# Kernel tuning notes

Hardware: AMD Instinct MI355X
Metric: run time of the kernel (lower is better)

Reference implementation:

```python
import jax, jax.numpy as jnp
import numpy as np

N_TABLES = 26
VOCAB = 100000
D = 64          # m_spa
B = 16384
L = 4           # fixed pooling factor (uniform offsets)
LN_BOT = [13, 512, 256, 64]
LN_TOP = [415, 512, 256, 1]


def setup_inputs() -> dict:
    key = jax.random.key(0)
    ks = jax.random.split(key, 20)
    inp = {}
    inp["dense_x"] = jax.random.uniform(ks[0], (B, LN_BOT[0]), dtype=jnp.float32)
    # offsets: uniform bags of length L (EmbeddingBag offsets per table)
    inp["lS_o"] = jnp.tile(jnp.arange(B, dtype=jnp.int64) * L, (N_TABLES, 1))
    inp["lS_i"] = jax.random.randint(ks[1], (N_TABLES, B * L), 0, VOCAB, dtype=jnp.int64)
    # embedding tables, uniform(-sqrt(1/n), sqrt(1/n)) as in create_emb
    bound = np.sqrt(1.0 / VOCAB)
    inp["emb"] = jax.random.uniform(ks[2], (N_TABLES, VOCAB, D), dtype=jnp.float32,
                                     minval=-bound, maxval=bound)
    # MLP params, normal init as in create_mlp
    def mk_mlp(ln, k0):
        Ws, bs = [], []
        for i in range(len(ln) - 1):
            n, m = ln[i], ln[i + 1]
            kw, kb = jax.random.split(jax.random.fold_in(k0, i))
            Ws.append(jax.random.normal(kw, (m, n), dtype=jnp.float32) * np.sqrt(2.0 / (m + n)))
            bs.append(jax.random.normal(kb, (m,), dtype=jnp.float32) * np.sqrt(1.0 / m))
        return Ws, bs
    bW, bb = mk_mlp(LN_BOT, ks[3])
    tW, tb = mk_mlp(LN_TOP, ks[4])
    for i in range(3):
        inp[f"bot_W{i}"], inp[f"bot_b{i}"] = bW[i], bb[i]
        inp[f"top_W{i}"], inp[f"top_b{i}"] = tW[i], tb[i]
    return inp


def _lower_tri_pairs(n):
    # li/lj from interact_features with offset=0: all (i, j) with j < i
    li = np.array([i for i in range(n) for j in range(i)])
    lj = np.array([j for i in range(n) for j in range(i)])
    return li, lj


def dlrm_forward(dense_x, lS_i, emb, bot_W, bot_b, top_W, top_b):
    # bottom MLP: Linear + ReLU (sigmoid_bot = -1)
    x = dense_x
    for W, b in zip(bot_W, bot_b):
        x = jax.nn.relu(x @ W.T + b)
    # EmbeddingBag sum pooling: gather rows then sum over bag (fixed L)
    idx = lS_i.reshape(N_TABLES, B, L)                 # [T,B,L]
    # vmap over tables: emb[t][idx[t]] -> [B,L,D] -> sum -> [B,D]
    ly = jax.vmap(lambda tbl, ix: tbl[ix].sum(axis=1))(emb, idx)  # [T,B,D]
    # dot interaction: T = [x] + ly along feature axis -> [B, 1+T, D]
    Tmat = jnp.concatenate([x[:, None, :], jnp.transpose(ly, (1, 0, 2))], axis=1)
    Z = jnp.einsum("bid,bjd->bij", Tmat, Tmat)         # [B, 27, 27]
    li, lj = _lower_tri_pairs(Tmat.shape[1])
    Zflat = Z[:, li, lj]                                # [B, 351]
    R = jnp.concatenate([x, Zflat], axis=1)             # [B, 415]
    # top MLP: ReLU, ReLU, Sigmoid (sigmoid_top = 2)
    z = R
    for i, (W, b) in enumerate(zip(top_W, top_b)):
        z = z @ W.T + b
        z = jax.nn.sigmoid(z) if i == len(top_W) - 1 else jax.nn.relu(z)
    return z  # loss_threshold == 0 -> no clamp


def reference(dense_x, lS_o, lS_i, emb,
              bot_W0, bot_b0, bot_W1, bot_b1, bot_W2, bot_b2,
              top_W0, top_b0, top_W1, top_b1, top_W2, top_b2):
    # lS_o encodes uniform bags of length L; structure is honored via reshape.
    del lS_o
    return dlrm_forward(dense_x, lS_i, emb,
                        [bot_W0, bot_W1, bot_W2], [bot_b0, bot_b1, bot_b2],
                        [top_W0, top_W1, top_W2], [top_b0, top_b1, top_b2])
```

## Files before the change

### kernel.cpp

```cpp
#include <hip/hip_runtime.h>
#include <hip/hip_bf16.h>
#include <cmath>

#define BATCH   16384
#define NT      26
#define VOCAB_N 100000
#define EMB_D   64
#define LOOK    4

typedef __attribute__((ext_vector_type(8))) short  short8;
typedef __attribute__((ext_vector_type(4))) float  float4v;

#define GLOBAL_AS __attribute__((address_space(1)))
#define LDS_AS    __attribute__((address_space(3)))

static __device__ __forceinline__ short f32_to_bf16_bits(float f) {
    unsigned u = __builtin_bit_cast(unsigned, f);
    unsigned r = (u + 0x7fffu + ((u >> 16) & 1u)) >> 16;
    return (short)r;
}
static __device__ __forceinline__ float bf16_bits_to_f32(short s) {
    return __builtin_bit_cast(float, ((unsigned)(unsigned short)s) << 16);
}

__global__ __launch_bounds__(256) void conv_all(
    const float* __restrict__ bW1, const float* __restrict__ bW2,
    const float* __restrict__ tW0, const float* __restrict__ tW1,
    __hip_bfloat16* __restrict__ wb1, __hip_bfloat16* __restrict__ wb2,
    __hip_bfloat16* __restrict__ wt0, __hip_bfloat16* __restrict__ wt1)
{
    int i = blockIdx.x * 256 + threadIdx.x;
    if (i < 131072) { wb1[i] = __float2bfloat16(bW1[i]); return; }
    i -= 131072;
    if (i < 16384)  { wb2[i] = __float2bfloat16(bW2[i]); return; }
    i -= 16384;
    if (i < 212992) {
        int r = i / 416, k = i % 416;
        wt0[i] = __float2bfloat16(k < 415 ? tW0[(size_t)r * 415 + k] : 0.f);
        return;
    }
    i -= 212992;
    if (i < 131072) wt1[i] = __float2bfloat16(tW1[i]);
}

__global__ __launch_bounds__(256) void gemm_f32_k13(
    const float* __restrict__ X, const float* __restrict__ W,
    const float* __restrict__ bias, __hip_bfloat16* __restrict__ Y,
    int M, int N, int K)
{
    constexpr int BM = 128, BN = 128, BK = 16, TM = 8, TN = 8, PAD = 4;
    __shared__ __align__(16) float Xs[BK][BM + PAD];
    __shared__ __align__(16) float Ws[BK][BN + PAD];

    const int tid = threadIdx.x;
    const int tx  = tid % (BN / TN);
    const int ty  = tid / (BN / TN);
    const int m0  = blockIdx.y * BM;
    const int n0  = blockIdx.x * BN;

    float acc[TM][TN];
    #pragma unroll
    for (int i = 0; i < TM; i++)
        #pragma unroll
        for (int j = 0; j < TN; j++) acc[i][j] = 0.f;

    for (int k0 = 0; k0 < K; k0 += BK) {
        for (int idx = tid; idx < BM * BK; idx += 256) {
            int r = idx / BK, k = idx % BK, gk = k0 + k;
            Xs[k][r] = (gk < K) ? X[(size_t)(m0 + r) * K + gk] : 0.f;
        }
        for (int idx = tid; idx < BN * BK; idx += 256) {
            int r = idx / BK, k = idx % BK, gk = k0 + k;
            Ws[k][r] = (gk < K) ? W[(size_t)(n0 + r) * K + gk] : 0.f;
        }
        __syncthreads();
        #pragma unroll
        for (int kk = 0; kk < BK; kk++) {
            float a[TM], bb[TN];
            #pragma unroll
            for (int i = 0; i < TM; i++) a[i] = Xs[kk][ty * TM + i];
            #pragma unroll
            for (int j = 0; j < TN; j++) bb[j] = Ws[kk][tx * TN + j];
            #pragma unroll
            for (int i = 0; i < TM; i++)
                #pragma unroll
                for (int j = 0; j < TN; j++)
                    acc[i][j] += a[i] * bb[j];
        }
        __syncthreads();
    }
    #pragma unroll
    for (int i = 0; i < TM; i++) {
        int m = m0 + ty * TM + i;
        #pragma unroll
        for (int j = 0; j < TN; j++) {
            int n = n0 + tx * TN + j;
            float v = fmaxf(acc[i][j] + bias[n], 0.f);
            Y[(size_t)m * N + n] = __float2bfloat16(v);
        }
    }
}

template<int BN, int WM, int WN, int RELU, int OUT_BF16>
__global__ __launch_bounds__(256) void mfma_gemm(
    const short* __restrict__ A, const short* __restrict__ W,
    const float* __restrict__ bias, void* __restrict__ Y,
    int M, int N, int K)
{
    constexpr int BM = 128, BK = 32;
    constexpr int FM = BM / WM / 16;
    constexpr int FN = BN / WN / 16;
    constexpr int ACH = (BM * BK * 2) / 1024;
    constexpr int BCH = (BN * BK * 2) / 1024;

    __shared__ short As[BM * BK];
    __shared__ short Bs[BN * BK];

    const int tid  = threadIdx.x;
    const int wave = tid >> 6;
    const int lane = tid & 63;
    const int wm   = wave / WN;
    const int wn   = wave % WN;
    const int m0   = blockIdx.y * BM;
    const int n0   = blockIdx.x * BN;

    const int r16 = lane >> 2;
    const int c16 = (lane & 3) * 8;

    float4v acc[FM][FN];
    #pragma unroll
    for (int i = 0; i < FM; i++)
        #pragma unroll
        for (int j = 0; j < FN; j++) acc[i][j] = (float4v)(0.f);

    for (int k0 = 0; k0 < K; k0 += BK) {
        #pragma unroll
        for (int c = 0; c < ACH / 4; c++) {
            int chunk = wave * (ACH / 4) + c;
            int row   = chunk * 16 + r16;
            const short* src = A + (size_t)(m0 + row) * K + k0 + c16;
            __builtin_amdgcn_global_load_lds(
                (const GLOBAL_AS void*)src,
                (LDS_AS void*)(As + chunk * 512), 16, 0, 0);
        }
        #pragma unroll
        for (int c = 0; c < BCH / 4; c++) {
            int chunk = wave * (BCH / 4) + c;
            int row   = chunk * 16 + r16;
            const short* src = W + (size_t)(n0 + row) * K + k0 + c16;
            __builtin_amdgcn_global_load_lds(
                (const GLOBAL_AS void*)src,
                (LDS_AS void*)(Bs + chunk * 512), 16, 0, 0);
        }
        __syncthreads();

        short8 a_frag[FM], b_frag[FN];
        const int kq = (lane >> 4) * 8;
        #pragma unroll
        for (int fi = 0; fi < FM; fi++) {
            int m_local = wm * (BM / WM) + fi * 16 + (lane & 15);
            a_frag[fi] = *(const short8*)(As + m_local * BK + kq);
        }
        #pragma unroll
        for (int fj = 0; fj < FN; fj++) {
            int n_local = wn * (BN / WN) + fj * 16 + (lane & 15);
            b_frag[fj] = *(const short8*)(Bs + n_local * BK + kq);
        }
        #pragma unroll
        for (int fi = 0; fi < FM; fi++)
            #pragma unroll
            for (int fj = 0; fj < FN; fj++)
                acc[fi][fj] = __builtin_amdgcn_mfma_f32_16x16x32_bf16(
                    a_frag[fi], b_frag[fj], acc[fi][fj], 0, 0, 0);

        __syncthreads();
    }

    #pragma unroll
    for (int fi = 0; fi < FM; fi++) {
        #pragma unroll
        for (int fj = 0; fj < FN; fj++) {
            int col   = n0 + wn * (BN / WN) + fj * 16 + (lane & 15);
            int rbase = m0 + wm * (BM / WM) + fi * 16 + (lane >> 4) * 4;
            float bv  = bias[col];
            #pragma unroll
            for (int r = 0; r < 4; r++) {
                float v = acc[fi][fj][r] + bv;
                if (RELU) v = fmaxf(v, 0.f);
                if (OUT_BF16)
                    ((__hip_bfloat16*)Y)[(size_t)(rbase + r) * N + col] =
                        __float2bfloat16(v);
                else
                    ((float*)Y)[(size_t)(rbase + r) * N + col] = v;
            }
        }
    }
}

#define TS 68

__global__ __launch_bounds__(256) void interact_kernel(
    const float* __restrict__ x2,
    const int*   __restrict__ lS_i,
    const float* __restrict__ emb,
    __hip_bfloat16* __restrict__ R)
{
    __shared__ __align__(16) float T[32 * TS];
    __shared__ int sidx[NT * LOOK];

    const int b   = blockIdx.x;
    const int tid = threadIdx.x;

    if (tid < NT * LOOK) {
        int tb = tid >> 2, l = tid & 3;
        sidx[tid] = lS_i[(size_t)tb * (BATCH * LOOK) + (size_t)b * LOOK + l];
    }
    if (tid < 16) {
        *(float4*)(&T[tid * 4]) = *(const float4*)(x2 + (size_t)b * EMB_D + tid * 4);
    }
    for (int i = 27 * TS + tid; i < 32 * TS; i += 256) T[i] = 0.f;
    __syncthreads();

    const int c4 = (tid & 15) * 4;
    #pragma unroll
    for (int it = 0; it < 2; ++it) {
        int tb = (tid >> 4) + it * 16;
        if (tb < NT) {
            float4 s = {0.f, 0.f, 0.f, 0.f};
            #pragma unroll
            for (int l = 0; l < LOOK; l++) {
                int row = sidx[tb * LOOK + l];
                float4 v = *(const float4*)(emb +
                    ((size_t)tb * VOCAB_N + row) * EMB_D + c4);
                s.x += v.x; s.y += v.y; s.z += v.z; s.w += v.w;
            }
            *(float4*)(&T[(tb + 1) * TS + c4]) = s;
        }
    }
    __syncthreads();

    const int wave = tid >> 6;
    const int lane = tid & 63;
    __hip_bfloat16* Rb = R + (size_t)b * 416;

    if (wave < 3) {
        const int ti = (wave == 0) ? 0 : 1;
        const int tj = (wave == 2) ? 1 : 0;

        short8 fhi[2][2], flo[2][2];
        const int r  = lane & 15;
        const int kq = (lane >> 4) * 8;
        #pragma unroll
        for (int rt = 0; rt < 2; rt++) {
            #pragma unroll
            for (int kk = 0; kk < 2; kk++) {
                const float* src = &T[(rt * 16 + r) * TS + kk * 32 + kq];
                float4 v0 = *(const float4*)(src);
                float4 v1 = *(const float4*)(src + 4);
                float vv[8] = {v0.x, v0.y, v0.z, v0.w, v1.x, v1.y, v1.z, v1.w};
                short8 h, l;
                #pragma unroll
                for (int j = 0; j < 8; j++) {
                    short hb = f32_to_bf16_bits(vv[j]);
                    float hf = bf16_bits_to_f32(hb);
                    short lb = f32_to_bf16_bits(vv[j] - hf);
                    h[j] = hb; l[j] = lb;
                }
                fhi[rt][kk] = h; flo[rt][kk] = l;
            }
        }

        float4v acc = (float4v)(0.f);
        #pragma unroll
        for (int kk = 0; kk < 2; kk++) {
            acc = __builtin_amdgcn_mfma_f32_16x16x32_bf16(
                      fhi[ti][kk], fhi[tj][kk], acc, 0, 0, 0);
            acc = __builtin_amdgcn_mfma_f32_16x16x32_bf16(
                      fhi[ti][kk], flo[tj][kk], acc, 0, 0, 0);
            acc = __builtin_amdgcn_mfma_f32_16x16x32_bf16(
                      flo[ti][kk], fhi[tj][kk], acc, 0, 0, 0);
        }

        const int gj = tj * 16 + (lane & 15);
        #pragma unroll
        for (int rr = 0; rr < 4; rr++) {
            int gi = ti * 16 + (lane >> 4) * 4 + rr;
            if (gi < NT + 1 && gi > gj) {
                int p = gi * (gi - 1) / 2 + gj;
                Rb[64 + p] = __float2bfloat16(acc[rr]);
            }
        }
    } else {
        Rb[lane] = __float2bfloat16(T[lane]);
        if (lane == 0) Rb[415] = __float2bfloat16(0.f);
    }
}

__global__ __launch_bounds__(256) void top_final(
    const float* __restrict__ z1, const float* __restrict__ W2,
    const float* __restrict__ b2, float* __restrict__ out)
{
    const int wave = threadIdx.x >> 6;
    const int lane = threadIdx.x & 63;
    const int b = blockIdx.x * 4 + wave;

    float s = 0.f;
    #pragma unroll
    for (int q = 0; q < 4; q++) {
        int k = q * 64 + lane;
        s += z1[(size_t)b * 256 + k] * W2[k];
    }
    #pragma unroll
    for (int off = 32; off; off >>= 1) s += __shfl_down(s, off, 64);
    if (lane == 0) out[b] = 1.f / (1.f + expf(-(s + b2[0])));
}

extern "C" void kernel_launch(void* const* d_in, const int* in_sizes, int n_in,
                              void* d_out, int out_size, void* d_ws, size_t ws_size,
                              hipStream_t stream)
{
    const float* dense = (const float*)d_in[0];
    const int*   lS_i  = (const int*)d_in[2];
    const float* emb   = (const float*)d_in[3];
    const float* bW0 = (const float*)d_in[4];  const float* bb0 = (const float*)d_in[5];
    const float* tW0 = (const float*)d_in[6];  const float* tb0 = (const float*)d_in[7];
    const float* bW1 = (const float*)d_in[8];  const float* bb1 = (const float*)d_in[9];
    const float* tW1 = (const float*)d_in[10]; const float* tb1 = (const float*)d_in[11];
    const float* bW2 = (const float*)d_in[12]; const float* bb2 = (const float*)d_in[13];
    const float* tW2 = (const float*)d_in[14]; const float* tb2 = (const float*)d_in[15];
    float* out = (float*)d_out;

    char* p = (char*)d_ws;
    __hip_bfloat16* x0_bf = (__hip_bfloat16*)p;  p += (size_t)BATCH * 512 * 2;
    __hip_bfloat16* x1_bf = (__hip_bfloat16*)p;  p += (size_t)BATCH * 256 * 2;
    float*          x2_f  = (float*)p;           p += (size_t)BATCH * 64  * 4;
    __hip_bfloat16* R_bf  = (__hip_bfloat16*)p;  p += (size_t)BATCH * 416 * 2;
    __hip_bfloat16* z0_bf = (__hip_bfloat16*)p;  p += (size_t)BATCH * 512 * 2;
    float*          z1_f  = (float*)p;           p += (size_t)BATCH * 256 * 4;
    __hip_bfloat16* wb1   = (__hip_bfloat16*)p;  p += (size_t)256 * 512 * 2;
    __hip_bfloat16* wb2   = (__hip_bfloat16*)p;  p += (size_t)64  * 256 * 2;
    __hip_bfloat16* wt0   = (__hip_bfloat16*)p;  p += (size_t)512 * 416 * 2;
    __hip_bfloat16* wt1   = (__hip_bfloat16*)p;  p += (size_t)256 * 512 * 2;

    dim3 blk(256);

    conv_all<<<dim3(1920), blk, 0, stream>>>(bW1, bW2, tW0, tW1, wb1, wb2, wt0, wt1);

    gemm_f32_k13<<<dim3(512 / 128, BATCH / 128), blk, 0, stream>>>(
        dense, bW0, bb0, x0_bf, BATCH, 512, 13);
    mfma_gemm<128, 2, 2, 1, 1><<<dim3(256 / 128, BATCH / 128), blk, 0, stream>>>(
        (const short*)x0_bf, (const short*)wb1, bb1, x1_bf, BATCH, 256, 512);
    mfma_gemm<64, 4, 1, 1, 0><<<dim3(1, BATCH / 128), blk, 0, stream>>>(
        (const short*)x1_bf, (const short*)wb2, bb2, x2_f, BATCH, 64, 256);

    interact_kernel<<<dim3(BATCH), blk, 0, stream>>>(x2_f, lS_i, emb, R_bf);

    mfma_gemm<128, 2, 2, 1, 1><<<dim3(512 / 128, BATCH / 128), blk, 0, stream>>>(
        (const short*)R_bf, (const short*)wt0, tb0, z0_bf, BATCH, 512, 416);
    mfma_gemm<128, 2, 2, 1, 0><<<dim3(256 / 128, BATCH / 128), blk, 0, stream>>>(
        (const short*)z0_bf, (const short*)wt1, tb1, z1_f, BATCH, 256, 512);
    top_final<<<dim3(BATCH / 4), blk, 0, stream>>>(z1_f, tW2, tb2, out);
}
```

Baseline: 895.9 us.

## Fuse bottom-MLP last layer into interaction and top layer 1 into final

```diff
diff --git a/kernel.cpp b/kernel.cpp
--- a/kernel.cpp
+++ b/kernel.cpp
@@ -200,13 +200,17 @@
 #define TS 68
 
 __global__ __launch_bounds__(256) void interact_kernel(
-    const float* __restrict__ x2,
+    const short* __restrict__ x1,
+    const short* __restrict__ wb2,
+    const float* __restrict__ bb2,
     const int*   __restrict__ lS_i,
     const float* __restrict__ emb,
     __hip_bfloat16* __restrict__ R)
 {
     __shared__ __align__(16) float T[32 * TS];
     __shared__ int sidx[NT * LOOK];
+    __shared__ __align__(16) short x1row[256];
+    __shared__ __align__(16) float red[64][4];
 
     const int b   = blockIdx.x;
     const int tid = threadIdx.x;
@@ -215,27 +219,67 @@
         int tb = tid >> 2, l = tid & 3;
         sidx[tid] = lS_i[(size_t)tb * (BATCH * LOOK) + (size_t)b * LOOK + l];
     }
-    if (tid < 16) {
-        *(float4*)(&T[tid * 4]) = *(const float4*)(x2 + (size_t)b * EMB_D + tid * 4);
+    if (tid >= 128 && tid < 160) {
+        int o = (tid - 128) * 8;
+        *(short8*)(&x1row[o]) = *(const short8*)(x1 + (size_t)b * 256 + o);
     }
     for (int i = 27 * TS + tid; i < 32 * TS; i += 256) T[i] = 0.f;
     __syncthreads();
 
-    const int c4 = (tid & 15) * 4;
-    #pragma unroll
-    for (int it = 0; it < 2; ++it) {
-        int tb = (tid >> 4) + it * 16;
-        if (tb < NT) {
-            float4 s = {0.f, 0.f, 0.f, 0.f};
-            #pragma unroll
-            for (int l = 0; l < LOOK; l++) {
-                int row = sidx[tb * LOOK + l];
-                float4 v = *(const float4*)(emb +
-                    ((size_t)tb * VOCAB_N + row) * EMB_D + c4);
-                s.x += v.x; s.y += v.y; s.z += v.z; s.w += v.w;
-            }
-            *(float4*)(&T[(tb + 1) * TS + c4]) = s;
-        }
+    const int c4  = (tid & 15) * 4;
+    const int tb0 = tid >> 4;
+    const int tb1 = tb0 + 16;
+    float4 g[8];
+    #pragma unroll
+    for (int l = 0; l < LOOK; l++) {
+        int row = sidx[tb0 * LOOK + l];
+        g[l] = *(const float4*)(emb + ((size_t)tb0 * VOCAB_N + row) * EMB_D + c4);
+    }
+    if (tb1 < NT) {
+        #pragma unroll
+        for (int l = 0; l < LOOK; l++) {
+            int row = sidx[tb1 * LOOK + l];
+            g[4 + l] = *(const float4*)(emb + ((size_t)tb1 * VOCAB_N + row) * EMB_D + c4);
+        }
+    }
+
+    {
+        const int d = tid & 63, q = tid >> 6;
+        const short* wrow = wb2 + d * 256 + q * 64;
+        float p = 0.f;
+        #pragma unroll
+        for (int c = 0; c < 8; c++) {
+            short8 w  = *(const short8*)(wrow + c * 8);
+            short8 xv = *(const short8*)(&x1row[q * 64 + c * 8]);
+            #pragma unroll
+            for (int j = 0; j < 8; j++)
+                p += bf16_bits_to_f32(xv[j]) * bf16_bits_to_f32(w[j]);
+        }
+        red[d][q] = p;
+    }
+
+    {
+        float4 s = g[0];
+        s.x += g[1].x + g[2].x + g[3].x;
+        s.y += g[1].y + g[2].y + g[3].y;
+        s.z += g[1].z + g[2].z + g[3].z;
+        s.w += g[1].w + g[2].w + g[3].w;
+        *(float4*)(&T[(tb0 + 1) * TS + c4]) = s;
+        if (tb1 < NT) {
+            float4 t = g[4];
+            t.x += g[5].x + g[6].x + g[7].x;
+            t.y += g[5].y + g[6].y + g[7].y;
+            t.z += g[5].z + g[6].z + g[7].z;
+            t.w += g[5].w + g[6].w + g[7].w;
+            *(float4*)(&T[(tb1 + 1) * TS + c4]) = t;
+        }
+    }
+    __syncthreads();
+
+    if (tid < 64) {
+        float4 r4 = *(const float4*)(&red[tid][0]);
+        float v = r4.x + r4.y + r4.z + r4.w + bb2[tid];
+        T[tid] = fmaxf(v, 0.f);
     }
     __syncthreads();
 
@@ -296,23 +340,99 @@
     }
 }
 
-__global__ __launch_bounds__(256) void top_final(
-    const float* __restrict__ z1, const float* __restrict__ W2,
-    const float* __restrict__ b2, float* __restrict__ out)
-{
-    const int wave = threadIdx.x >> 6;
-    const int lane = threadIdx.x & 63;
-    const int b = blockIdx.x * 4 + wave;
-
-    float s = 0.f;
-    #pragma unroll
-    for (int q = 0; q < 4; q++) {
-        int k = q * 64 + lane;
-        s += z1[(size_t)b * 256 + k] * W2[k];
-    }
-    #pragma unroll
-    for (int off = 32; off; off >>= 1) s += __shfl_down(s, off, 64);
-    if (lane == 0) out[b] = 1.f / (1.f + expf(-(s + b2[0])));
+__global__ __launch_bounds__(256) void top1_final(
+    const short* __restrict__ A,
+    const short* __restrict__ W,
+    const float* __restrict__ bias,
+    const float* __restrict__ W2,
+    const float* __restrict__ b2,
+    float* __restrict__ out)
+{
+    constexpr int BM = 64, BN = 256, BK = 32, K = 512;
+    __shared__ short As[BM * BK];
+    __shared__ short Bs[BN * BK];
+    __shared__ __align__(16) float red[64][4];
+
+    const int tid  = threadIdx.x;
+    const int wave = tid >> 6;
+    const int lane = tid & 63;
+    const int m0   = blockIdx.x * BM;
+
+    const int r16 = lane >> 2;
+    const int c16 = (lane & 3) * 8;
+
+    float4v acc[4][4];
+    #pragma unroll
+    for (int i = 0; i < 4; i++)
+        #pragma unroll
+        for (int j = 0; j < 4; j++) acc[i][j] = (float4v)(0.f);
+
+    for (int k0 = 0; k0 < K; k0 += BK) {
+        {
+            int row = wave * 16 + r16;
+            const short* src = A + (size_t)(m0 + row) * K + k0 + c16;
+            __builtin_amdgcn_global_load_lds(
+                (const GLOBAL_AS void*)src,
+                (LDS_AS void*)(As + wave * 512), 16, 0, 0);
+        }
+        #pragma unroll
+        for (int c = 0; c < 4; c++) {
+            int chunk = wave * 4 + c;
+            int row   = chunk * 16 + r16;
+            const short* src = W + (size_t)row * K + k0 + c16;
+            __builtin_amdgcn_global_load_lds(
+                (const GLOBAL_AS void*)src,
+                (LDS_AS void*)(Bs + chunk * 512), 16, 0, 0);
+        }
+        __syncthreads();
+
+        short8 a_frag[4], b_frag[4];
+        const int kq = (lane >> 4) * 8;
+        #pragma unroll
+        for (int fi = 0; fi < 4; fi++) {
+            int m_local = fi * 16 + (lane & 15);
+            a_frag[fi] = *(const short8*)(As + m_local * BK + kq);
+        }
+        #pragma unroll
+        for (int fj = 0; fj < 4; fj++) {
+            int n_local = wave * 64 + fj * 16 + (lane & 15);
+            b_frag[fj] = *(const short8*)(Bs + n_local * BK + kq);
+        }
+        #pragma unroll
+        for (int fi = 0; fi < 4; fi++)
+            #pragma unroll
+            for (int fj = 0; fj < 4; fj++)
+                acc[fi][fj] = __builtin_amdgcn_mfma_f32_16x16x32_bf16(
+                    a_frag[fi], b_frag[fj], acc[fi][fj], 0, 0, 0);
+
+        __syncthreads();
+    }
+
+    #pragma unroll
+    for (int fi = 0; fi < 4; fi++) {
+        #pragma unroll
+        for (int rr = 0; rr < 4; rr++) {
+            float s = 0.f;
+            #pragma unroll
+            for (int fj = 0; fj < 4; fj++) {
+                int col = wave * 64 + fj * 16 + (lane & 15);
+                float v = fmaxf(acc[fi][fj][rr] + bias[col], 0.f);
+                s += v * W2[col];
+            }
+            s += __shfl_xor(s, 1, 64);
+            s += __shfl_xor(s, 2, 64);
+            s += __shfl_xor(s, 4, 64);
+            s += __shfl_xor(s, 8, 64);
+            if ((lane & 15) == 0)
+                red[fi * 16 + (lane >> 4) * 4 + rr][wave] = s;
+        }
+    }
+    __syncthreads();
+    if (tid < 64) {
+        float4 r4 = *(const float4*)(&red[tid][0]);
+        float s = r4.x + r4.y + r4.z + r4.w + b2[0];
+        out[m0 + tid] = 1.f / (1.f + expf(-s));
+    }
 }
 
 extern "C" void kernel_launch(void* const* d_in, const int* in_sizes, int n_in,
@@ -333,10 +453,8 @@
     char* p = (char*)d_ws;
     __hip_bfloat16* x0_bf = (__hip_bfloat16*)p;  p += (size_t)BATCH * 512 * 2;
     __hip_bfloat16* x1_bf = (__hip_bfloat16*)p;  p += (size_t)BATCH * 256 * 2;
-    float*          x2_f  = (float*)p;           p += (size_t)BATCH * 64  * 4;
     __hip_bfloat16* R_bf  = (__hip_bfloat16*)p;  p += (size_t)BATCH * 416 * 2;
     __hip_bfloat16* z0_bf = (__hip_bfloat16*)p;  p += (size_t)BATCH * 512 * 2;
-    float*          z1_f  = (float*)p;           p += (size_t)BATCH * 256 * 4;
     __hip_bfloat16* wb1   = (__hip_bfloat16*)p;  p += (size_t)256 * 512 * 2;
     __hip_bfloat16* wb2   = (__hip_bfloat16*)p;  p += (size_t)64  * 256 * 2;
     __hip_bfloat16* wt0   = (__hip_bfloat16*)p;  p += (size_t)512 * 416 * 2;
@@ -350,14 +468,13 @@
         dense, bW0, bb0, x0_bf, BATCH, 512, 13);
     mfma_gemm<128, 2, 2, 1, 1><<<dim3(256 / 128, BATCH / 128), blk, 0, stream>>>(
         (const short*)x0_bf, (const short*)wb1, bb1, x1_bf, BATCH, 256, 512);
-    mfma_gemm<64, 4, 1, 1, 0><<<dim3(1, BATCH / 128), blk, 0, stream>>>(
-        (const short*)x1_bf, (const short*)wb2, bb2, x2_f, BATCH, 64, 256);
-
-    interact_kernel<<<dim3(BATCH), blk, 0, stream>>>(x2_f, lS_i, emb, R_bf);
+
+    interact_kernel<<<dim3(BATCH), blk, 0, stream>>>(
+        (const short*)x1_bf, (const short*)wb2, bb2, lS_i, emb, R_bf);
 
     mfma_gemm<128, 2, 2, 1, 1><<<dim3(512 / 128, BATCH / 128), blk, 0, stream>>>(
         (const short*)R_bf, (const short*)wt0, tb0, z0_bf, BATCH, 512, 416);
-    mfma_gemm<128, 2, 2, 1, 0><<<dim3(256 / 128, BATCH / 128), blk, 0, stream>>>(
-        (const short*)z0_bf, (const short*)wt1, tb1, z1_f, BATCH, 256, 512);
-    top_final<<<dim3(BATCH / 4), blk, 0, stream>>>(z1_f, tW2, tb2, out);
-}
+
+    top1_final<<<dim3(BATCH / 64), blk, 0, stream>>>(
+        (const short*)z0_bf, (const short*)wt1, tb1, tW2, tb2, out);
+}
```

New measurement: 964.3 us. 1.08x slower.
